# Performance work log

Measured on AMD Instinct MI355X. Metric: run time of the kernel, lower is better.

Reference implementation:

```python
import jax, jax.numpy as jnp
import numpy as np

G_SPARSITY = 1.0

def _w16_to_4():
    W = np.zeros((4, 16), dtype=np.float32)
    W[0, 8:16] = 1
    W[1, [2, 3, 6, 7]] = 1
    W[1, [8, 9, 12, 13]] = -1
    W[2, [4, 5, 6, 7]] = 1
    W[2, [8, 9, 10, 11]] = -1
    W[3, 1] = 1
    W[3, 6] = -2
    W[3, [2, 4, 7, 14]] = -1
    W[3, [1, 8, 11, 13]] = 1
    W[3, 9] = 2
    return jnp.asarray(W)

W16_TO_4 = _w16_to_4()

def setup_inputs() -> dict:
    key = jax.random.key(0)
    k1, k2 = jax.random.split(key)
    N = 65536
    batch = 256
    x = jax.random.uniform(k1, (batch, 2 * N), dtype=jnp.float32)
    w = jax.random.normal(k2, (16, N), dtype=jnp.float32)
    return {"x": x, "w": w}

def reference(x, w):
    batch = x.shape[0]
    N = w.shape[1]
    xg = x.reshape(batch, N, 2)
    A = xg[:, :, 0]  # (batch, N)
    B = xg[:, :, 1]
    weights = jax.nn.softmax(w * G_SPARSITY, axis=0)       # (16, N)
    wc = jnp.matmul(W16_TO_4, weights)                      # (4, N)
    # sum over the 4 basis functions {1, A, B, A*B}
    out = wc[0] + wc[1] * A + wc[2] * B + wc[3] * (A * B)   # (batch, N)
    return out
```

## Files before the change

kernel.cpp:

```cpp
#include <hip/hip_runtime.h>

#define NCOLS 65536
#define BATCH 256
#define TOTAL4 (BATCH * NCOLS / 4)

typedef float f32x4 __attribute__((ext_vector_type(4)));

__global__ void gate_precompute(const float* __restrict__ w, float* __restrict__ wc) {
    int n = blockIdx.x * blockDim.x + threadIdx.x;
    float e[16];
    float m = -INFINITY;
#pragma unroll
    for (int j = 0; j < 16; ++j) {
        e[j] = w[j * NCOLS + n];
        m = fmaxf(m, e[j]);
    }
    float s = 0.f;
#pragma unroll
    for (int j = 0; j < 16; ++j) {
        e[j] = __expf(e[j] - m);
        s += e[j];
    }
    float inv = 1.0f / s;
    float c0 = (e[8] + e[9] + e[10] + e[11] + e[12] + e[13] + e[14] + e[15]) * inv;
    float c1 = (e[2] + e[3] + e[6] + e[7] - e[8] - e[9] - e[12] - e[13]) * inv;
    float c2 = (e[4] + e[5] + e[6] + e[7] - e[8] - e[9] - e[10] - e[11]) * inv;
    float c3 = (e[1] - e[2] - e[4] - 2.f * e[6] - e[7] + e[8] + 2.f * e[9] + e[11] + e[13] - e[14]) * inv;
    wc[0 * NCOLS + n] = c0;
    wc[1 * NCOLS + n] = c1;
    wc[2 * NCOLS + n] = c2;
    wc[3 * NCOLS + n] = c3;
}

__global__ __launch_bounds__(256) void gate_apply(const f32x4* __restrict__ x4,
                                                  const f32x4* __restrict__ wc4,
                                                  f32x4* __restrict__ out4) {
    int stride = gridDim.x * blockDim.x;
    for (int i = blockIdx.x * blockDim.x + threadIdx.x; i < TOTAL4; i += stride) {
        int b  = i >> 14;
        int n4 = i & 16383;
        const f32x4* xp = x4 + ((size_t)b << 15) + ((size_t)n4 << 1);
        f32x4 x0 = __builtin_nontemporal_load(xp);
        f32x4 x1 = __builtin_nontemporal_load(xp + 1);
        f32x4 c0 = wc4[0 * 16384 + n4];
        f32x4 c1 = wc4[1 * 16384 + n4];
        f32x4 c2 = wc4[2 * 16384 + n4];
        f32x4 c3 = wc4[3 * 16384 + n4];
        f32x4 a = {x0.x, x0.z, x1.x, x1.z};
        f32x4 bv = {x0.y, x0.w, x1.y, x1.w};
        f32x4 o = c0 + c1 * a + c2 * bv + c3 * (a * bv);
        __builtin_nontemporal_store(o, out4 + i);
    }
}

extern "C" void kernel_launch(void* const* d_in, const int* in_sizes, int n_in,
                              void* d_out, int out_size, void* d_ws, size_t ws_size,
                              hipStream_t stream) {
    const float* x = (const float*)d_in[0];
    const float* w = (const float*)d_in[1];
    float* out = (float*)d_out;
    float* wc = (float*)d_ws;

    gate_precompute<<<NCOLS / 256, 256, 0, stream>>>(w, wc);

    gate_apply<<<2048, 256, 0, stream>>>((const f32x4*)x, (const f32x4*)wc, (f32x4*)out);
}
```

Before: 215.7 us.

## Fuse softmax gate precompute into apply kernel with shared-memory coefficients

Merges the coefficient precompute and the apply pass into one kernel. Each block computes the softmax-derived coefficients for a 512-column tile into shared memory, then applies them to 16 batch rows. This removes a kernel launch and the global workspace round trip for the coefficients. In exchange, the softmax over w is recomputed once per row chunk, adding redundant w reads and exp work.

```diff
diff --git a/kernel.cpp b/kernel.cpp
--- a/kernel.cpp
+++ b/kernel.cpp
@@ -2,54 +2,63 @@
 
 #define NCOLS 65536
 #define BATCH 256
-#define TOTAL4 (BATCH * NCOLS / 4)
+#define CPB 512
+#define RPB 16
 
 typedef float f32x4 __attribute__((ext_vector_type(4)));
 
-__global__ void gate_precompute(const float* __restrict__ w, float* __restrict__ wc) {
-    int n = blockIdx.x * blockDim.x + threadIdx.x;
-    float e[16];
-    float m = -INFINITY;
+__global__ __launch_bounds__(256) void gate_fused(const float* __restrict__ x,
+                                                  const float* __restrict__ w,
+                                                  float* __restrict__ out) {
+    __shared__ float wcs[4][CPB];
+    const int tid = threadIdx.x;
+    const int col_tile = blockIdx.x & 127;
+    const int row_chunk = blockIdx.x >> 7;
+    const int c0 = col_tile * CPB;
+    const int r0 = row_chunk * RPB;
+
 #pragma unroll
-    for (int j = 0; j < 16; ++j) {
-        e[j] = w[j * NCOLS + n];
-        m = fmaxf(m, e[j]);
+    for (int p = 0; p < 2; ++p) {
+        int c = c0 + p * 256 + tid;
+        float e[16];
+        float m = -INFINITY;
+#pragma unroll
+        for (int j = 0; j < 16; ++j) {
+            e[j] = w[j * NCOLS + c];
+            m = fmaxf(m, e[j]);
+        }
+        float s = 0.f;
+#pragma unroll
+        for (int j = 0; j < 16; ++j) {
+            e[j] = __expf(e[j] - m);
+            s += e[j];
+        }
+        float inv = 1.0f / s;
+        int lc = p * 256 + tid;
+        wcs[0][lc] = (e[8] + e[9] + e[10] + e[11] + e[12] + e[13] + e[14] + e[15]) * inv;
+        wcs[1][lc] = (e[2] + e[3] + e[6] + e[7] - e[8] - e[9] - e[12] - e[13]) * inv;
+        wcs[2][lc] = (e[4] + e[5] + e[6] + e[7] - e[8] - e[9] - e[10] - e[11]) * inv;
+        wcs[3][lc] = (e[1] - e[2] - e[4] - 2.f * e[6] - e[7] + e[8] + 2.f * e[9] + e[11] + e[13] - e[14]) * inv;
     }
-    float s = 0.f;
+    __syncthreads();
+
+    const int g = tid & 127;
+    const int rhalf = tid >> 7;
+    f32x4 c0v = *(const f32x4*)&wcs[0][g * 4];
+    f32x4 c1v = *(const f32x4*)&wcs[1][g * 4];
+    f32x4 c2v = *(const f32x4*)&wcs[2][g * 4];
+    f32x4 c3v = *(const f32x4*)&wcs[3][g * 4];
+
 #pragma unroll
-    for (int j = 0; j < 16; ++j) {
-        e[j] = __expf(e[j] - m);
-        s += e[j];
-    }
-    float inv = 1.0f / s;
-    float c0 = (e[8] + e[9] + e[10] + e[11] + e[12] + e[13] + e[14] + e[15]) * inv;
-    float c1 = (e[2] + e[3] + e[6] + e[7] - e[8] - e[9] - e[12] - e[13]) * inv;
-    float c2 = (e[4] + e[5] + e[6] + e[7] - e[8] - e[9] - e[10] - e[11]) * inv;
-    float c3 = (e[1] - e[2] - e[4] - 2.f * e[6] - e[7] + e[8] + 2.f * e[9] + e[11] + e[13] - e[14]) * inv;
-    wc[0 * NCOLS + n] = c0;
-    wc[1 * NCOLS + n] = c1;
-    wc[2 * NCOLS + n] = c2;
-    wc[3 * NCOLS + n] = c3;
-}
-
-__global__ __launch_bounds__(256) void gate_apply(const f32x4* __restrict__ x4,
-                                                  const f32x4* __restrict__ wc4,
-                                                  f32x4* __restrict__ out4) {
-    int stride = gridDim.x * blockDim.x;
-    for (int i = blockIdx.x * blockDim.x + threadIdx.x; i < TOTAL4; i += stride) {
-        int b  = i >> 14;
-        int n4 = i & 16383;
-        const f32x4* xp = x4 + ((size_t)b << 15) + ((size_t)n4 << 1);
+    for (int it = 0; it < 8; ++it) {
+        int r = r0 + rhalf + it * 2;
+        const f32x4* xp = (const f32x4*)(x + (size_t)r * (2 * NCOLS) + (size_t)(c0 * 2 + g * 8));
         f32x4 x0 = __builtin_nontemporal_load(xp);
         f32x4 x1 = __builtin_nontemporal_load(xp + 1);
-        f32x4 c0 = wc4[0 * 16384 + n4];
-        f32x4 c1 = wc4[1 * 16384 + n4];
-        f32x4 c2 = wc4[2 * 16384 + n4];
-        f32x4 c3 = wc4[3 * 16384 + n4];
-        f32x4 a = {x0.x, x0.z, x1.x, x1.z};
+        f32x4 a  = {x0.x, x0.z, x1.x, x1.z};
         f32x4 bv = {x0.y, x0.w, x1.y, x1.w};
-        f32x4 o = c0 + c1 * a + c2 * bv + c3 * (a * bv);
-        __builtin_nontemporal_store(o, out4 + i);
+        f32x4 o = c0v + c1v * a + c2v * bv + c3v * (a * bv);
+        __builtin_nontemporal_store(o, (f32x4*)(out + (size_t)r * NCOLS + c0 + g * 4));
     }
 }
 
@@ -59,9 +68,7 @@
     const float* x = (const float*)d_in[0];
     const float* w = (const float*)d_in[1];
     float* out = (float*)d_out;
-    float* wc = (float*)d_ws;
+    (void)d_ws; (void)ws_size;
 
-    gate_precompute<<<NCOLS / 256, 256, 0, stream>>>(w, wc);
-
-    gate_apply<<<2048, 256, 0, stream>>>((const f32x4*)x, (const f32x4*)wc, (f32x4*)out);
+    gate_fused<<<(NCOLS / CPB) * (BATCH / RPB), 256, 0, stream>>>(x, w, out);
 }
```

Result: faster. 207.1 us (-4.0%).
